# Kernel tuning notes

Measured on AMD Instinct MI355X. Metric: run time of the kernel, lower is better.

The kernel has to match this reference:

```python
import jax, jax.numpy as jnp
import numpy as np

N_SERIES = 1024  # N; x carries 3N stacked time-synchronous nodes
GCN_DEPTH = 2
IN_DIM = 64
H_DIM = 64


def setup_inputs() -> dict:
    key = jax.random.key(0)
    k = jax.random.split(key, 6)
    B, C, N3 = 64, IN_DIM, 3 * N_SERIES
    x = jax.random.normal(k[0], (N3, B, C), dtype=jnp.float32)
    A = jax.random.normal(k[1], (N3, N3), dtype=jnp.float32) * 0.02
    # Linear2d (1x1 conv) params per depth; act='glu' -> out = 2*h_dim
    s0 = 1.0 / np.sqrt(IN_DIM)
    s1 = 1.0 / np.sqrt(H_DIM)
    W0 = jax.random.uniform(k[2], (2 * H_DIM, IN_DIM), jnp.float32, -s0, s0)
    b0 = jax.random.uniform(k[3], (2 * H_DIM,), jnp.float32, -s0, s0)
    W1 = jax.random.uniform(k[4], (2 * H_DIM, H_DIM), jnp.float32, -s1, s1)
    b1 = jax.random.uniform(k[5], (2 * H_DIM,), jnp.float32, -s1, s1)
    return {"x": x, "A": A, "W0": W0, "b0": b0, "W1": W1, "b1": b1}


def reference(x, A, W0, b0, W1, b1):
    # x: (3N, B, C) -> (B, C, 3N)
    h = jnp.transpose(x, (1, 2, 0))
    convs = []
    for W, b in ((W0, b0), (W1, b1)):
        # GCN2d flow='tgt_to_src': h[b,c,v] = sum_w h[b,c,w] * A[v,w]  (L=1 squeezed)
        g = jnp.einsum('bcw,vw->bcv', h, A)
        # Linear2d 1x1 conv: channels C -> 2*h_dim, then GLU gate
        y = jnp.einsum('oc,bcv->bov', W, g) + b[None, :, None]
        lhs, rhs = jnp.split(y, 2, axis=1)
        h = lhs * jax.nn.sigmoid(rhs)          # (B, h_dim, 3N)
        convs.append(jnp.transpose(h, (2, 0, 1)))  # (3N, B, h_dim)
    # crop the middle N nodes of each depth, then max over depth
    cropped = jnp.stack([c[N_SERIES:2 * N_SERIES] for c in convs], axis=0)
    return jnp.max(cropped, axis=0)  # (N, B, h_dim)
```

## Files before the change

kernel.cpp:

```cpp
#include <hip/hip_runtime.h>
#include <hip/hip_bf16.h>
#include <stdint.h>

typedef __attribute__((ext_vector_type(8))) short s16x8;
typedef __attribute__((ext_vector_type(4))) float f32x4;
typedef __attribute__((ext_vector_type(8))) unsigned short u16x8;
typedef __attribute__((ext_vector_type(4))) unsigned short u16x4;

__device__ __forceinline__ float bf2f(unsigned short u) {
  union { uint32_t u; float f; } v; v.u = ((uint32_t)u) << 16; return v.f;
}
__device__ __forceinline__ unsigned short f2bf(float f) {
  union { float f; uint32_t u; } v; v.f = f;
  uint32_t u = v.u;
  return (unsigned short)((u + 0x7fffu + ((u >> 16) & 1u)) >> 16);
}
__device__ __forceinline__ void load_lds16(const void* g, void* l) {
  __builtin_amdgcn_global_load_lds(
      (const __attribute__((address_space(1))) void*)g,
      (__attribute__((address_space(3))) void*)l, 16, 0, 0);
}


__global__ void k_detect(const uint32_t* __restrict__ xw, int* __restrict__ flag) {
  int lane = threadIdx.x;
  uint32_t u = xw[lane * 97 + 1];
  int e = (u >> 7) & 0xFF;
  unsigned long long m = __ballot(e > 150);
  if (lane == 0) *flag = (__popcll(m) > 6) ? 1 : 0;
}

__global__ __launch_bounds__(256) void k_transpose(const void* __restrict__ xin,
                                                   unsigned short* __restrict__ xtp,
                                                   const int* __restrict__ flag) {
  __shared__ __align__(16) unsigned short tile[64 * 65];
  const int t = threadIdx.x;
  const int w0 = blockIdx.x * 64;
  const int m0 = blockIdx.y * 64;
  if (*flag) {
    const float* xf = (const float*)xin;
#pragma unroll
    for (int rep = 0; rep < 4; ++rep) {
      int vi = t + rep * 256;
      int r = vi >> 4;
      int c4 = (vi & 15) * 4;
      f32x4 v = *(const f32x4*)(xf + (uint64_t)(w0 + r) * 4096 + m0 + c4);
#pragma unroll
      for (int u = 0; u < 4; ++u) tile[(c4 + u) * 65 + r] = f2bf(v[u]);
    }
  } else {
    const unsigned short* xb = (const unsigned short*)xin;
#pragma unroll
    for (int rep = 0; rep < 2; ++rep) {
      int vi = t + rep * 256;
      int r = vi >> 3;
      int c8 = (vi & 7) * 8;
      u16x8 v = *(const u16x8*)(xb + (uint64_t)(w0 + r) * 4096 + m0 + c8);
#pragma unroll
      for (int u = 0; u < 8; ++u) tile[(c8 + u) * 65 + r] = v[u];
    }
  }
  __syncthreads();
  unsigned short* dst = xtp + ((uint64_t)(m0 >> 6) * 48 + (w0 >> 6)) * 4096;
#pragma unroll
  for (int rep = 0; rep < 2; ++rep) {
    int vi = t + rep * 256;
    int kb = vi >> 6, r = vi & 63;
    u16x8 v;
#pragma unroll
    for (int u = 0; u < 8; ++u) v[u] = tile[r * 65 + kb * 8 + u];
    *(u16x8*)(dst + kb * 512 + r * 8) = v;
  }
}

__global__ __launch_bounds__(256) void k_packA(const void* __restrict__ Ain,
                                               unsigned short* __restrict__ Abp,
                                               const int* __restrict__ flag) {
  __shared__ __align__(16) unsigned short tl[8 * 520];
  const int t = threadIdx.x;
  const int kt = blockIdx.x, rt = blockIdx.y;
  if (*flag) {
    const float* Af = (const float*)Ain;
#pragma unroll
    for (int rep = 0; rep < 4; ++rep) {
      int vi = t + rep * 256;
      int r = vi >> 4;
      int c4 = (vi & 15) * 4;
      f32x4 v = *(const f32x4*)(Af + (uint64_t)(rt * 64 + r) * 3072 + kt * 64 + c4);
      int kb = c4 >> 3, e = c4 & 7;
#pragma unroll
      for (int u = 0; u < 4; ++u) tl[kb * 520 + r * 8 + e + u] = f2bf(v[u]);
    }
  } else {
    const unsigned short* Ab16 = (const unsigned short*)Ain;
#pragma unroll
    for (int rep = 0; rep < 2; ++rep) {
      int vi = t + rep * 256;
      int r = vi >> 3;
      int c8 = (vi & 7) * 8;
      u16x8 v = *(const u16x8*)(Ab16 + (uint64_t)(rt * 64 + r) * 3072 + kt * 64 + c8);
#pragma unroll
      for (int u = 0; u < 8; ++u) tl[(c8 >> 3) * 520 + r * 8 + u] = v[u];
    }
  }
  __syncthreads();
  unsigned short* dst = Abp + ((uint64_t)rt * 48 + kt) * 4096;
#pragma unroll
  for (int rep = 0; rep < 2; ++rep) {
    int vi = t + rep * 256;
    int kb = vi >> 6, r = vi & 63;
    u16x8 v;
#pragma unroll
    for (int u = 0; u < 8; ++u) v[u] = tl[kb * 520 + r * 8 + u];
    *(u16x8*)(dst + kb * 512 + r * 8) = v;
  }
}

__global__ __launch_bounds__(256) void k_cvtW(const void* __restrict__ W0,
                                              const void* __restrict__ b0,
                                              const void* __restrict__ W1,
                                              const void* __restrict__ b1,
                                              unsigned short* __restrict__ wb,
                                              const int* __restrict__ flag) {
  int fp = *flag;
  for (int i = threadIdx.x; i < 16640; i += 256) {
    const void* src; int off;
    if (i < 8192)        { src = W0; off = i; }
    else if (i < 8320)   { src = b0; off = i - 8192; }
    else if (i < 16512)  { src = W1; off = i - 8320; }
    else                 { src = b1; off = i - 16512; }
    wb[i] = fp ? f2bf(((const float*)src)[off]) : ((const unsigned short*)src)[off];
  }
}

template <int BM>
__global__ __launch_bounds__(256) void k_gemm_glu(const unsigned short* __restrict__ Am,
                                                  const unsigned short* __restrict__ Bm,
                                                  const unsigned short* __restrict__ W,
                                                  const unsigned short* __restrict__ bias,
                                                  unsigned short* __restrict__ H,
                                                  int K, int Vtot) {
  constexpr int IF = BM / 32;
  constexpr int VPW = BM / 64;
  constexpr int NTA = BM / 64;
  constexpr int NT = NTA + 2;
  constexpr int STAGE = NT * 4096;
  constexpr int GTILE = BM * 136;
  constexpr int SME = STAGE > GTILE ? STAGE : GTILE;
  __shared__ __align__(16) unsigned short smem[SME];

  const int t = threadIdx.x;
  const int lane = t & 63;
  const int wid = t >> 6;
  const int wV = wid >> 1;
  const int wM = wid & 1;
  const int v0 = blockIdx.x * BM;
  const int m0 = blockIdx.y * 128;
  const int Kt = K >> 6;

  f32x4 acc[IF][4] = {};

  const unsigned short* tbase = nullptr;
  if (wid < NT) {
    tbase = (wid < NTA)
                ? Am + ((uint64_t)((v0 >> 6) + wid) * Kt) * 4096
                : Bm + ((uint64_t)((m0 >> 6) + (wid - NTA)) * Kt) * 4096;
    tbase += lane * 8;
  }
  unsigned short* lbase = smem + wid * 4096;

  const int fr = lane & 15;
  const int q4 = lane >> 4;

  for (int kt = 0; kt < Kt; ++kt) {
    __syncthreads();
    if (wid < NT) {
      const unsigned short* src = tbase + (uint64_t)kt * 4096;
#pragma unroll
      for (int q = 0; q < 8; ++q)
        load_lds16(src + q * 512, lbase + q * 512);
    }
    __syncthreads();
#pragma unroll
    for (int ks = 0; ks < 64; ks += 32) {
      const int kb = (ks >> 3) + q4;
      s16x8 af[IF], bf[4];
#pragma unroll
      for (int i = 0; i < IF; ++i) {
        int row = wV * (BM / 2) + i * 16 + fr;
        af[i] = *(const s16x8*)(smem + (row >> 6) * 4096 + kb * 512 + (row & 63) * 8);
      }
#pragma unroll
      for (int j = 0; j < 4; ++j) {
        int row = wM * 64 + j * 16 + fr;
        bf[j] = *(const s16x8*)(smem + (NTA + (row >> 6)) * 4096 + kb * 512 + (row & 63) * 8);
      }
#pragma unroll
      for (int i = 0; i < IF; ++i)
#pragma unroll
        for (int j = 0; j < 4; ++j)
          acc[i][j] = __builtin_amdgcn_mfma_f32_16x16x32_bf16(af[i], bf[j], acc[i][j], 0, 0, 0);
    }
  }

  __syncthreads();
  {
    const int rr = q4 * 4;
#pragma unroll
    for (int i = 0; i < IF; ++i)
#pragma unroll
      for (int j = 0; j < 4; ++j) {
        int col = wM * 64 + j * 16 + fr;
#pragma unroll
        for (int r = 0; r < 4; ++r) {
          int row = wV * (BM / 2) + i * 16 + rr + r;
          smem[row * 136 + col] = f2bf(acc[i][j][r]);
        }
      }
  }
  __syncthreads();

  s16x8 wf[2][8];
#pragma unroll
  for (int ksi = 0; ksi < 2; ++ksi)
#pragma unroll
    for (int j = 0; j < 8; ++j)
      wf[ksi][j] = *(const s16x8*)(W + (j * 16 + fr) * 64 + ksi * 32 + q4 * 8);
  float bj[8];
#pragma unroll
  for (int j = 0; j < 8; ++j) bj[j] = bf2f(bias[j * 16 + fr]);

  const int Vt = Vtot >> 6;
#pragma unroll
  for (int b = 0; b < 2; ++b) {
    f32x4 acc2[VPW][8] = {};
#pragma unroll
    for (int vv = 0; vv < VPW; ++vv)
#pragma unroll
      for (int ksi = 0; ksi < 2; ++ksi) {
        s16x8 af = *(const s16x8*)(smem + ((wid * VPW + vv) * 16 + fr) * 136 +
                                   b * 64 + ksi * 32 + q4 * 8);
#pragma unroll
        for (int j = 0; j < 8; ++j)
          acc2[vv][j] = __builtin_amdgcn_mfma_f32_16x16x32_bf16(af, wf[ksi][j], acc2[vv][j], 0, 0, 0);
      }
#pragma unroll
    for (int vv = 0; vv < VPW; ++vv) {
      int v = v0 + (wid * VPW + vv) * 16 + q4 * 4;
#pragma unroll
      for (int j = 0; j < 4; ++j) {
        u16x4 pk;
#pragma unroll
        for (int r = 0; r < 4; ++r) {
          float lhs = acc2[vv][j][r] + bj[j];
          float rhs = acc2[vv][j + 4][r] + bj[j + 4];
          float sg = 1.0f / (1.0f + __expf(-rhs));
          pk[r] = f2bf(lhs * sg);
        }
        int o = j * 16 + fr;
        int hrow = m0 + b * 64 + o;
        *(u16x4*)(H + ((uint64_t)(hrow >> 6) * Vt + (v >> 6)) * 4096 +
                  ((v >> 3) & 7) * 512 + o * 8 + (v & 7)) = pk;
      }
    }
  }
}

__global__ __launch_bounds__(256) void k_maxout(const unsigned short* __restrict__ H1,
                                                const unsigned short* __restrict__ H2,
                                                float* __restrict__ out) {
  __shared__ __align__(16) float tile[64 * 65];
  const int t = threadIdx.x;
  const int b = blockIdx.y;
  const int n0 = blockIdx.x * 64;
  {
    int j = t >> 2, p = t & 3;
    int c1 = 1024 + n0 + p * 16;
    int c2 = n0 + p * 16;
    const unsigned short* h1p =
        H1 + ((uint64_t)b * 48 + (c1 >> 6)) * 4096 + ((c1 >> 3) & 7) * 512 + j * 8;
    const unsigned short* h2p =
        H2 + ((uint64_t)b * 16 + (c2 >> 6)) * 4096 + ((c2 >> 3) & 7) * 512 + j * 8;
    u16x8 a0 = *(const u16x8*)(h1p);
    u16x8 a1 = *(const u16x8*)(h1p + 512);
    u16x8 c0 = *(const u16x8*)(h2p);
    u16x8 c1v = *(const u16x8*)(h2p + 512);
#pragma unroll
    for (int u = 0; u < 8; ++u) {
      tile[j * 65 + p * 16 + u] = fmaxf(bf2f(a0[u]), bf2f(c0[u]));
      tile[j * 65 + p * 16 + 8 + u] = fmaxf(bf2f(a1[u]), bf2f(c1v[u]));
    }
  }
  __syncthreads();
  {
    int n = t >> 2, jb = (t & 3) * 16;
    float* op = out + (uint64_t)(n0 + n) * 4096 + b * 64 + jb;
#pragma unroll
    for (int q = 0; q < 4; ++q) {
      f32x4 o;
#pragma unroll
      for (int u = 0; u < 4; ++u) o[u] = tile[(jb + q * 4 + u) * 65 + n];
      *(f32x4*)(op + q * 4) = o;
    }
  }
}

extern "C" void kernel_launch(void* const* d_in, const int* in_sizes, int n_in,
                              void* d_out, int out_size, void* d_ws, size_t ws_size,
                              hipStream_t stream) {
  (void)in_sizes; (void)n_in; (void)out_size; (void)ws_size;
  const void* x  = d_in[0];
  const void* A  = d_in[1];
  const void* W0 = d_in[2];
  const void* b0 = d_in[3];
  const void* W1 = d_in[4];
  const void* b1 = d_in[5];
  float* out = (float*)d_out;

  char* ws = (char*)d_ws;
  unsigned short* Xtp = (unsigned short*)(ws + 0);
  unsigned short* H2p = (unsigned short*)(ws + 0);
  unsigned short* Abp = (unsigned short*)(ws + 25165824);
  unsigned short* Wb  = (unsigned short*)(ws + 44040192);
  unsigned short* H1p = (unsigned short*)(ws + 44105728);
  int* flag = (int*)(ws + 69271552);

  k_detect<<<1, 64, 0, stream>>>((const uint32_t*)x, flag);
  k_transpose<<<dim3(48, 64), 256, 0, stream>>>(x, Xtp, flag);
  k_packA<<<dim3(48, 48), 256, 0, stream>>>(A, Abp, flag);
  k_cvtW<<<1, 256, 0, stream>>>(W0, b0, W1, b1, Wb, flag);
  k_gemm_glu<128><<<dim3(24, 32), 256, 0, stream>>>(Abp, Xtp, Wb, Wb + 8192, H1p, 3072, 3072);
  k_gemm_glu<64><<<dim3(16, 32), 256, 0, stream>>>(Abp + (uint64_t)16 * 48 * 4096, H1p,
                                                    Wb + 8320, Wb + 16512, H2p, 3072, 1024);
  k_maxout<<<dim3(16, 64), 256, 0, stream>>>(H1p, H2p, out);
}
```

Baseline: 315.5 us.

## Rewrite GCN GEMM with 4-stage LDS pipeline, 512 threads and larger tiles

Replaces the single-buffered GEMM+GLU kernel with a version that prefetches three K-slices ahead into a 4-deep LDS ring using global_load_lds. It waits on explicit vmcnt counts and raw s_barrier instead of double __syncthreads. Tiles grow to 192/128 x 256 with 8 waves per block, and MFMA issue is wrapped in setprio. The goal is to hide global-memory latency and raise MFMA utilisation and operand reuse. In exchange it uses fewer blocks (256 and 128), which risks under-filling the CUs, and it depends on hand-tuned waitcnt literals for correctness.

```diff
diff --git a/kernel.cpp b/kernel.cpp
--- a/kernel.cpp
+++ b/kernel.cpp
@@ -20,6 +20,9 @@
       (const __attribute__((address_space(1))) void*)g,
       (__attribute__((address_space(3))) void*)l, 16, 0, 0);
 }
+
+#define VMW(n) asm volatile("s_waitcnt vmcnt(" #n ")" ::: "memory")
+#define SBAR() asm volatile("s_barrier" ::: "memory")
 
 
 __global__ void k_detect(const uint32_t* __restrict__ xw, int* __restrict__ flag) {
@@ -133,88 +136,138 @@
   }
 }
 
-template <int BM>
-__global__ __launch_bounds__(256) void k_gemm_glu(const unsigned short* __restrict__ Am,
-                                                  const unsigned short* __restrict__ Bm,
-                                                  const unsigned short* __restrict__ W,
-                                                  const unsigned short* __restrict__ bias,
-                                                  unsigned short* __restrict__ H,
-                                                  int K, int Vtot) {
-  constexpr int IF = BM / 32;
-  constexpr int VPW = BM / 64;
-  constexpr int NTA = BM / 64;
-  constexpr int NT = NTA + 2;
-  constexpr int STAGE = NT * 4096;
-  constexpr int GTILE = BM * 136;
-  constexpr int SME = STAGE > GTILE ? STAGE : GTILE;
+template <int BM, int KTOT>
+__global__ __launch_bounds__(512, 2) void k_gemm_glu2(
+    const unsigned short* __restrict__ Am,
+    const unsigned short* __restrict__ Bm,
+    const unsigned short* __restrict__ W,
+    const unsigned short* __restrict__ bias,
+    unsigned short* __restrict__ H,
+    int Vtot) {
+  constexpr int BN  = 256;
+  constexpr int IF  = BM / 32;
+  constexpr int NPH = (IF > 4) ? 2 : 1;
+  constexpr int IPH = IF / NPH;
+  constexpr int APL = (BM / 64) * 4;
+  constexpr int P   = APL + 16;
+  constexpr int QF  = P / 8;
+  constexpr int QR  = P - QF * 8;
+  constexpr int PPW = QF + (QR ? 1 : 0);
+  constexpr int BUFS = P * 512;
+  constexpr int NT  = KTOT / 32;
+  constexpr int Kt  = KTOT / 64;
+  constexpr int NRB = BM / 16;
+  constexpr int EPL = BM * 264;
+  constexpr int SME = (4 * BUFS > EPL) ? 4 * BUFS : EPL;
+  static_assert(QF == 3, "vmcnt literals below assume QF==3");
+
   __shared__ __align__(16) unsigned short smem[SME];
 
-  const int t = threadIdx.x;
+  const int t    = threadIdx.x;
   const int lane = t & 63;
-  const int wid = t >> 6;
-  const int wV = wid >> 1;
-  const int wM = wid & 1;
-  const int v0 = blockIdx.x * BM;
-  const int m0 = blockIdx.y * 128;
-  const int Kt = K >> 6;
+  const int wid  = t >> 6;
+  const int wV   = wid >> 2;
+  const int wM   = wid & 3;
+  const int fr   = lane & 15;
+  const int q4   = lane >> 4;
+  const int v0   = blockIdx.x * BM;
+  const int m0   = blockIdx.y * BN;
+  const int art0 = v0 >> 6;
+  const int brt0 = m0 >> 6;
+
+  const int myq = QF + ((QR && wid < QR) ? 1 : 0);
+  const unsigned short* srcb[PPW];
+  int ldso[PPW];
+#pragma unroll
+  for (int q = 0; q < PPW; ++q) {
+    int pi = wid + 8 * q;
+    if (pi >= P) pi = P - 1;
+    const int isA = pi < APL;
+    const int rtl = (isA ? pi : pi - APL) >> 2;
+    const int pb  = pi & 3;
+    const unsigned short* base =
+        isA ? (Am + (uint64_t)(art0 + rtl) * Kt * 4096)
+            : (Bm + (uint64_t)(brt0 + rtl) * Kt * 4096);
+    srcb[q] = base + pb * 512 + lane * 8;
+    ldso[q] = pi * 512;
+  }
+
+  int aoff[IF], boff[4];
+#pragma unroll
+  for (int i = 0; i < IF; ++i) {
+    const int row = wV * (BM / 2) + i * 16 + fr;
+    aoff[i] = ((row >> 6) * 4 + q4) * 512 + (row & 63) * 8;
+  }
+#pragma unroll
+  for (int j = 0; j < 4; ++j)
+    boff[j] = (APL + wM * 4 + q4) * 512 + (j * 16 + fr) * 8;
 
   f32x4 acc[IF][4] = {};
 
-  const unsigned short* tbase = nullptr;
-  if (wid < NT) {
-    tbase = (wid < NTA)
-                ? Am + ((uint64_t)((v0 >> 6) + wid) * Kt) * 4096
-                : Bm + ((uint64_t)((m0 >> 6) + (wid - NTA)) * Kt) * 4096;
-    tbase += lane * 8;
-  }
-  unsigned short* lbase = smem + wid * 4096;
-
-  const int fr = lane & 15;
-  const int q4 = lane >> 4;
-
-  for (int kt = 0; kt < Kt; ++kt) {
-    __syncthreads();
-    if (wid < NT) {
-      const unsigned short* src = tbase + (uint64_t)kt * 4096;
-#pragma unroll
-      for (int q = 0; q < 8; ++q)
-        load_lds16(src + q * 512, lbase + q * 512);
-    }
-    __syncthreads();
-#pragma unroll
-    for (int ks = 0; ks < 64; ks += 32) {
-      const int kb = (ks >> 3) + q4;
-      s16x8 af[IF], bf[4];
-#pragma unroll
-      for (int i = 0; i < IF; ++i) {
-        int row = wV * (BM / 2) + i * 16 + fr;
-        af[i] = *(const s16x8*)(smem + (row >> 6) * 4096 + kb * 512 + (row & 63) * 8);
-      }
-#pragma unroll
-      for (int j = 0; j < 4; ++j) {
-        int row = wM * 64 + j * 16 + fr;
-        bf[j] = *(const s16x8*)(smem + (NTA + (row >> 6)) * 4096 + kb * 512 + (row & 63) * 8);
-      }
-#pragma unroll
-      for (int i = 0; i < IF; ++i)
+#pragma unroll
+  for (int pt = 0; pt < 3; ++pt)
+#pragma unroll
+    for (int q = 0; q < PPW; ++q)
+      if (q < myq)
+        load_lds16(srcb[q] + pt * 2048, smem + pt * BUFS + ldso[q]);
+  if (QR && wid < QR) { VMW(8); } else { VMW(6); }
+  SBAR();
+
+#pragma unroll 4
+  for (int tt = 0; tt < NT; ++tt) {
+    const unsigned short* buf = smem + (tt & 3) * BUFS;
+    s16x8 bfr[4];
+#pragma unroll
+    for (int ph = 0; ph < NPH; ++ph) {
+      if (ph == 0) {
 #pragma unroll
         for (int j = 0; j < 4; ++j)
-          acc[i][j] = __builtin_amdgcn_mfma_f32_16x16x32_bf16(af[i], bf[j], acc[i][j], 0, 0, 0);
-    }
-  }
-
-  __syncthreads();
+          bfr[j] = *(const s16x8*)(buf + boff[j]);
+      }
+      s16x8 afr[IPH];
+#pragma unroll
+      for (int ii = 0; ii < IPH; ++ii)
+        afr[ii] = *(const s16x8*)(buf + aoff[ph * IPH + ii]);
+      if (tt + 3 < NT) {
+        unsigned short* dst = smem + ((tt + 3) & 3) * BUFS;
+#pragma unroll
+        for (int q = 0; q < PPW; ++q)
+          if ((q % NPH) == ph && q < myq)
+            load_lds16(srcb[q] + (uint64_t)(tt + 3) * 2048, dst + ldso[q]);
+      }
+      SBAR();
+      __builtin_amdgcn_s_setprio(1);
+#pragma unroll
+      for (int ii = 0; ii < IPH; ++ii)
+#pragma unroll
+        for (int j = 0; j < 4; ++j)
+          acc[ph * IPH + ii][j] = __builtin_amdgcn_mfma_f32_16x16x32_bf16(
+              afr[ii], bfr[j], acc[ph * IPH + ii][j], 0, 0, 0);
+      __builtin_amdgcn_s_setprio(0);
+      if (ph == NPH - 1) {
+        if (tt + 3 < NT) {
+          if (QR && wid < QR) { VMW(8); } else { VMW(6); }
+        } else if (tt + 2 < NT) {
+          if (QR && wid < QR) { VMW(4); } else { VMW(3); }
+        } else {
+          VMW(0);
+        }
+      }
+      SBAR();
+    }
+  }
+
   {
     const int rr = q4 * 4;
 #pragma unroll
     for (int i = 0; i < IF; ++i)
 #pragma unroll
       for (int j = 0; j < 4; ++j) {
-        int col = wM * 64 + j * 16 + fr;
+        const int col = wM * 64 + j * 16 + fr;
 #pragma unroll
         for (int r = 0; r < 4; ++r) {
-          int row = wV * (BM / 2) + i * 16 + rr + r;
-          smem[row * 136 + col] = f2bf(acc[i][j][r]);
+          const int row = wV * (BM / 2) + i * 16 + rr + r;
+          smem[row * 264 + col] = f2bf(acc[i][j][r]);
         }
       }
   }
@@ -232,35 +285,37 @@
 
   const int Vt = Vtot >> 6;
 #pragma unroll
-  for (int b = 0; b < 2; ++b) {
-    f32x4 acc2[VPW][8] = {};
-#pragma unroll
-    for (int vv = 0; vv < VPW; ++vv)
-#pragma unroll
-      for (int ksi = 0; ksi < 2; ++ksi) {
-        s16x8 af = *(const s16x8*)(smem + ((wid * VPW + vv) * 16 + fr) * 136 +
-                                   b * 64 + ksi * 32 + q4 * 8);
-#pragma unroll
-        for (int j = 0; j < 8; ++j)
-          acc2[vv][j] = __builtin_amdgcn_mfma_f32_16x16x32_bf16(af, wf[ksi][j], acc2[vv][j], 0, 0, 0);
-      }
-#pragma unroll
-    for (int vv = 0; vv < VPW; ++vv) {
-      int v = v0 + (wid * VPW + vv) * 16 + q4 * 4;
-#pragma unroll
-      for (int j = 0; j < 4; ++j) {
-        u16x4 pk;
-#pragma unroll
-        for (int r = 0; r < 4; ++r) {
-          float lhs = acc2[vv][j][r] + bj[j];
-          float rhs = acc2[vv][j + 4][r] + bj[j + 4];
-          float sg = 1.0f / (1.0f + __expf(-rhs));
-          pk[r] = f2bf(lhs * sg);
+  for (int rep = 0; rep < (NRB + 7) / 8; ++rep) {
+    const int rb = rep * 8 + wid;
+    if (rb < NRB) {
+#pragma unroll
+      for (int bb = 0; bb < 4; ++bb) {
+        f32x4 acc2[8] = {};
+#pragma unroll
+        for (int ksi = 0; ksi < 2; ++ksi) {
+          s16x8 af = *(const s16x8*)(smem + (rb * 16 + fr) * 264 + bb * 64 +
+                                     ksi * 32 + q4 * 8);
+#pragma unroll
+          for (int j = 0; j < 8; ++j)
+            acc2[j] = __builtin_amdgcn_mfma_f32_16x16x32_bf16(af, wf[ksi][j],
+                                                              acc2[j], 0, 0, 0);
         }
-        int o = j * 16 + fr;
-        int hrow = m0 + b * 64 + o;
-        *(u16x4*)(H + ((uint64_t)(hrow >> 6) * Vt + (v >> 6)) * 4096 +
-                  ((v >> 3) & 7) * 512 + o * 8 + (v & 7)) = pk;
+        const int v = v0 + rb * 16 + q4 * 4;
+#pragma unroll
+        for (int j = 0; j < 4; ++j) {
+          u16x4 pk;
+#pragma unroll
+          for (int r = 0; r < 4; ++r) {
+            float lhs = acc2[j][r] + bj[j];
+            float rhs = acc2[j + 4][r] + bj[j + 4];
+            float sg = 1.0f / (1.0f + __expf(-rhs));
+            pk[r] = f2bf(lhs * sg);
+          }
+          const int o = j * 16 + fr;
+          const int hrow = m0 + bb * 64 + o;
+          *(u16x4*)(H + ((uint64_t)(hrow >> 6) * Vt + (v >> 6)) * 4096 +
+                    ((v >> 3) & 7) * 512 + (hrow & 63) * 8 + (v & 7)) = pk;
+        }
       }
     }
   }
@@ -329,8 +384,9 @@
   k_transpose<<<dim3(48, 64), 256, 0, stream>>>(x, Xtp, flag);
   k_packA<<<dim3(48, 48), 256, 0, stream>>>(A, Abp, flag);
   k_cvtW<<<1, 256, 0, stream>>>(W0, b0, W1, b1, Wb, flag);
-  k_gemm_glu<128><<<dim3(24, 32), 256, 0, stream>>>(Abp, Xtp, Wb, Wb + 8192, H1p, 3072, 3072);
-  k_gemm_glu<64><<<dim3(16, 32), 256, 0, stream>>>(Abp + (uint64_t)16 * 48 * 4096, H1p,
-                                                    Wb + 8320, Wb + 16512, H2p, 3072, 1024);
+  k_gemm_glu2<192, 3072><<<dim3(16, 16), 512, 0, stream>>>(
+      Abp, Xtp, Wb, Wb + 8192, H1p, 3072);
+  k_gemm_glu2<128, 3072><<<dim3(8, 16), 512, 0, stream>>>(
+      Abp + (uint64_t)16 * 48 * 4096, H1p, Wb + 8320, Wb + 16512, H2p, 1024);
   k_maxout<<<dim3(16, 64), 256, 0, stream>>>(H1p, H2p, out);
 }
```

New measurement: 299.7 us. -5.0%, faster.
